# Kernel optimization log

Hardware: AMD Instinct MI355X
Metric: run time of the kernel (lower is better)

## Reference

```python
import jax, jax.numpy as jnp
import numpy as np

N = 100000   # nodes
E = 1600000  # edges (avg degree 16)
DIN, DH, DOUT = 128, 128, 64


def setup_inputs() -> dict:
    key = jax.random.key(0)
    ks = jax.random.split(key, 10)
    x = jax.random.normal(ks[0], (N, DIN), dtype=jnp.float32)
    edge_index = jax.random.randint(ks[1], (2, E), 0, N, dtype=jnp.int32)

    def kaiming(k, fan_out, fan_in):
        # kaiming_uniform_ with nonlinearity='relu': bound = sqrt(6/fan_in)
        bound = np.sqrt(6.0 / fan_in)
        return jax.random.uniform(k, (fan_out, fan_in), jnp.float32, -bound, bound)

    W1 = kaiming(ks[2], DH, DIN)
    W2 = kaiming(ks[3], DH, DH)
    W3 = kaiming(ks[4], DH, DH)
    W4 = kaiming(ks[5], DOUT, DH)
    b1 = jnp.zeros((DH,), jnp.float32)
    b2 = jnp.zeros((DH,), jnp.float32)
    b3 = jnp.zeros((DH,), jnp.float32)
    b4 = jnp.zeros((DOUT,), jnp.float32)
    return {"x": x, "edge_index": edge_index,
            "W1": W1, "b1": b1, "W2": W2, "b2": b2,
            "W3": W3, "b3": b3, "W4": W4, "b4": b4}


def reference(x, edge_index, W1, b1, W2, b2, W3, b3, W4, b4):
    n = x.shape[0]
    src, dst = edge_index[0], edge_index[1]
    # gcn_norm with add_self_loops=False: deg = in-degree at dst (unit weights)
    deg = jax.ops.segment_sum(jnp.ones(src.shape[0], x.dtype), dst, num_segments=n)
    deg_inv_sqrt = jnp.where(deg > 0, jax.lax.rsqrt(jnp.maximum(deg, 1.0)) * jnp.sqrt(jnp.maximum(deg, 1.0)) / jnp.maximum(deg, 1.0) * jnp.sqrt(jnp.maximum(deg, 1.0)), 0.0)
    deg_inv_sqrt = jnp.where(deg > 0, 1.0 / jnp.sqrt(jnp.maximum(deg, 1.0)), 0.0)
    norm = deg_inv_sqrt[src] * deg_inv_sqrt[dst]  # [E]

    def gcn_layer(h, W, b):
        h = h @ W.T                                # [n, out] dense transform
        msg = h[src] * norm[:, None]               # gather + scale  [E, out]
        out = jax.ops.segment_sum(msg, dst, num_segments=n)  # scatter-add
        return out + b

    h = jax.nn.relu(gcn_layer(x, W1, b1))
    h = jax.nn.relu(gcn_layer(h, W2, b2))
    h = jax.nn.relu(gcn_layer(h, W3, b3))
    return gcn_layer(h, W4, b4)
```

## Files before the change

### kernel.cpp

```cpp
#include <hip/hip_runtime.h>
#include <hip/hip_bf16.h>

#define CAP 64
#define BCAP 250000
#define SBCAP 12288

typedef __attribute__((ext_vector_type(8))) short bf16x8;
typedef __attribute__((ext_vector_type(4))) float f32x4;
typedef _Float16 f16;
typedef __attribute__((ext_vector_type(2))) _Float16 f16x2;
typedef __attribute__((ext_vector_type(8))) _Float16 f16x8;

__device__ __forceinline__ ushort f2bf(float f) {
    uint u = __float_as_uint(f);
    u = u + 0x7FFF + ((u >> 16) & 1);
    return (ushort)(u >> 16);
}
__device__ __forceinline__ float bf2f(ushort b) { return __uint_as_float(((uint)b) << 16); }

__device__ __forceinline__ int bkt(int d, int r) {
    int b = 0;
    if (d >= 4 * r) b = 4;
    if (d >= (b + 2) * r) b += 2;
    if (d >= (b + 1) * r) b += 1;
    return b;
}

__global__ __launch_bounds__(256) void route_kernel(const int* __restrict__ src,
                                                    const int* __restrict__ dst,
                                                    int E, int N,
                                                    uint* __restrict__ buf,
                                                    int* __restrict__ gcur8) {
    __shared__ int lcnt[8], lbase[8];
    if (threadIdx.x < 8) lcnt[threadIdx.x] = 0;
    __syncthreads();
    const int r = (N + 7) >> 3;
    const int e = (blockIdx.x * 256 + threadIdx.x) * 4;
    int bb[4]; uint pk[4]; int ne = 0;
    if (e + 4 <= E) {
        int4 d4 = *(const int4*)(dst + e);
        int4 s4 = *(const int4*)(src + e);
        int ds[4] = {d4.x, d4.y, d4.z, d4.w};
        int ss[4] = {s4.x, s4.y, s4.z, s4.w};
#pragma unroll
        for (int k = 0; k < 4; ++k) {
            int b = bkt(ds[k], r);
            bb[k] = b;
            pk[k] = ((uint)ss[k] << 14) | (uint)(ds[k] - b * r);
            atomicAdd(&lcnt[b], 1);
        }
        ne = 4;
    } else {
        for (int t = e; t < E; ++t) {
            int b = bkt(dst[t], r);
            bb[ne] = b;
            pk[ne] = ((uint)src[t] << 14) | (uint)(dst[t] - b * r);
            atomicAdd(&lcnt[b], 1);
            ++ne;
        }
    }
    __syncthreads();
    if (threadIdx.x < 8) {
        lbase[threadIdx.x] = atomicAdd(&gcur8[threadIdx.x], lcnt[threadIdx.x]);
        lcnt[threadIdx.x] = 0;
    }
    __syncthreads();
    for (int k = 0; k < ne; ++k) {
        int idx = lbase[bb[k]] + atomicAdd(&lcnt[bb[k]], 1);
        if (idx < BCAP) buf[(size_t)bb[k] * BCAP + idx] = pk[k];
    }
}

__global__ __launch_bounds__(256) void reroute_kernel(const uint* __restrict__ buf,
                                                      const int* __restrict__ gcur8,
                                                      uint* __restrict__ buf2,
                                                      int* __restrict__ gcur2, int NSUB) {
    __shared__ int lcnt[32], lbase[32];
    const int xg = blockIdx.x & 7;
    const int gidx = blockIdx.x >> 3;
    if (threadIdx.x < NSUB) lcnt[threadIdx.x] = 0;
    __syncthreads();
    int cnt = gcur8[xg];
    if (cnt > BCAP) cnt = BCAP;
    const uint* b = buf + (size_t)xg * BCAP;
    const int e0 = (gidx * 256 + threadIdx.x) * 4;
    uint pk[4]; int sb_[4]; int ne = 0;
    if (e0 + 4 <= cnt) {
        uint4 v = *(const uint4*)(b + e0);
        pk[0] = v.x; pk[1] = v.y; pk[2] = v.z; pk[3] = v.w; ne = 4;
    } else {
        for (int t = e0; t < cnt; ++t) pk[ne++] = b[t];
    }
    for (int k = 0; k < ne; ++k) {
        int sub = (int)(pk[k] & 0x3FFFu) >> 9;
        sb_[k] = sub;
        atomicAdd(&lcnt[sub], 1);
    }
    __syncthreads();
    if (threadIdx.x < NSUB) {
        lbase[threadIdx.x] = atomicAdd(&gcur2[xg * NSUB + threadIdx.x], lcnt[threadIdx.x]);
        lcnt[threadIdx.x] = 0;
    }
    __syncthreads();
    for (int k = 0; k < ne; ++k) {
        int idx = lbase[sb_[k]] + atomicAdd(&lcnt[sb_[k]], 1);
        if (idx < SBCAP) buf2[(size_t)(xg * NSUB + sb_[k]) * SBCAP + idx] = pk[k];
    }
}

__global__ __launch_bounds__(256) void fillsort_kernel(const uint* __restrict__ buf2,
                                                       const int* __restrict__ gcur2,
                                                       int* __restrict__ fil,
                                                       int* __restrict__ csr, int N, int NSUB) {
    __shared__ uint stage[SBCAP];
    __shared__ int lcnt[512];
    const int xg = blockIdx.x & 7;
    const int sub = blockIdx.x >> 3;
    const int sb = xg * NSUB + sub;
    const int r = (N + 7) >> 3;
    const int lo_dl = sub << 9;
    const int ndst = min(512, r - lo_dl);
    if (ndst <= 0) return;
    int cnt = gcur2[sb];
    if (cnt > SBCAP) cnt = SBCAP;
    for (int i = threadIdx.x; i < cnt; i += 256) stage[i] = buf2[(size_t)sb * SBCAP + i];
    for (int i = threadIdx.x; i < ndst; i += 256) lcnt[i] = 0;
    __syncthreads();
    const int lo_d = xg * r + lo_dl;
    for (int i = threadIdx.x; i < cnt; i += 256) {
        uint pk = stage[i];
        int dll = (int)(pk & 0x3FFFu) - lo_dl;
        int s = (int)(pk >> 14);
        int p = atomicAdd(&lcnt[dll], 1);
        if (p < CAP) csr[(size_t)(lo_d + dll) * CAP + p] = s;
    }
    __syncthreads();
    for (int i = threadIdx.x; i < ndst; i += 256) {
        int d = lo_d + i;
        if (d < N) fil[d] = lcnt[i];
    }
}

__global__ void prep_kernel(const float* __restrict__ W1, const float* __restrict__ W2,
                            const float* __restrict__ W3, const float* __restrict__ W4,
                            ushort* __restrict__ hilo,
                            const int* __restrict__ cnt, float* __restrict__ dis, int N) {
    int blk = blockIdx.x;
    if (blk < 224) {
        int i = blk * 256 + threadIdx.x;
        const float* W;
        ushort* hi;
        int off;
        if (i < 16384)      { W = W1; hi = hilo;          off = i; }
        else if (i < 32768) { W = W2; hi = hilo + 32768;  off = i - 16384; }
        else if (i < 49152) { W = W3; hi = hilo + 65536;  off = i - 32768; }
        else                { W = W4; hi = hilo + 98304;  off = i - 49152; }
        float w = W[off];
        ushort h = f2bf(w);
        int span = (i < 49152) ? 16384 : 8192;
        hi[off] = h;
        hi[off + span] = f2bf(w - bf2f(h));
    } else {
        int i = (blk - 224) * 256 + threadIdx.x;
        if (i < N) {
            int c = cnt[i];
            dis[i] = (c > 0) ? rsqrtf((float)c) : 0.0f;
        }
    }
}

template <int COLS, typename FT>
__global__ __launch_bounds__(256) void mfma_gemm_kernel(const FT* __restrict__ F,
                                                        const ushort* __restrict__ Whi,
                                                        const ushort* __restrict__ Wlo,
                                                        const float* __restrict__ dis,
                                                        f16* __restrict__ G, int N) {
    constexpr int CT = COLS / 16;
    const int wave = threadIdx.x >> 6;
    const int lane = threadIdx.x & 63;
    const int lr = lane & 15;
    const int kg = lane >> 4;

    const int rowBase = blockIdx.x * 128 + wave * 32;

    f32x4 acc[2][CT];
#pragma unroll
    for (int rt = 0; rt < 2; ++rt)
#pragma unroll
        for (int c = 0; c < CT; ++c) acc[rt][c] = (f32x4){0.f, 0.f, 0.f, 0.f};

#pragma unroll
    for (int kt = 0; kt < 4; ++kt) {
        bf16x8 Ah[2], Al[2];
#pragma unroll
        for (int rt = 0; rt < 2; ++rt) {
            int row = rowBase + rt * 16 + lr;
            row = row < N ? row : N - 1;
            const FT* p = F + (size_t)row * 128 + kt * 32 + kg * 8;
            float f[8];
            if constexpr (sizeof(FT) == 4) {
                float4 v0 = *(const float4*)p;
                float4 v1 = *(const float4*)(p + 4);
                f[0] = v0.x; f[1] = v0.y; f[2] = v0.z; f[3] = v0.w;
                f[4] = v1.x; f[5] = v1.y; f[6] = v1.z; f[7] = v1.w;
            } else {
                f16x8 v = *(const f16x8*)p;
#pragma unroll
                for (int j = 0; j < 8; ++j) f[j] = (float)v[j];
            }
            bf16x8 h, l;
#pragma unroll
            for (int j = 0; j < 8; ++j) {
                ushort hb = f2bf(f[j]);
                h[j] = (short)hb;
                l[j] = (short)f2bf(f[j] - bf2f(hb));
            }
            Ah[rt] = h;
            Al[rt] = l;
        }
#pragma unroll
        for (int c = 0; c < CT; ++c) {
            const size_t wo = (size_t)(c * 16 + lr) * 128 + kt * 32 + kg * 8;
            bf16x8 Bh = *(const bf16x8*)(Whi + wo);
            bf16x8 Bl = *(const bf16x8*)(Wlo + wo);
#pragma unroll
            for (int rt = 0; rt < 2; ++rt) {
                acc[rt][c] = __builtin_amdgcn_mfma_f32_16x16x32_bf16(Al[rt], Bh, acc[rt][c], 0, 0, 0);
                acc[rt][c] = __builtin_amdgcn_mfma_f32_16x16x32_bf16(Ah[rt], Bl, acc[rt][c], 0, 0, 0);
                acc[rt][c] = __builtin_amdgcn_mfma_f32_16x16x32_bf16(Ah[rt], Bh, acc[rt][c], 0, 0, 0);
            }
        }
    }

#pragma unroll
    for (int rt = 0; rt < 2; ++rt) {
#pragma unroll
        for (int j = 0; j < 4; ++j) {
            int row = rowBase + rt * 16 + kg * 4 + j;
            if (row < N) {
                float d = dis[row];
#pragma unroll
                for (int c = 0; c < CT; ++c)
                    G[(size_t)row * COLS + c * 16 + lr] = (f16)(acc[rt][c][j] * d);
            }
        }
    }
}

template <int WIDTH, bool DO_RELU, typename OT>
__global__ __launch_bounds__(256) void agg_kernel(const f16* __restrict__ g,
                                                  const int* __restrict__ csr,
                                                  const int* __restrict__ cnt,
                                                  const float* __restrict__ dis,
                                                  const float* __restrict__ bias,
                                                  OT* __restrict__ out, int N) {
    constexpr int VPL = WIDTH / 64;
    const int nb8 = gridDim.x >> 3;
    const int vblk = (blockIdx.x & 7) * nb8 + (blockIdx.x >> 3);
    int node = vblk * 4 + (threadIdx.x >> 6);
    if (node >= N) return;
    int lane = threadIdx.x & 63;

    int c = cnt[node];
    if (c > CAP) c = CAP;
    const int* lst = csr + (size_t)node * CAP;
    float acc0 = 0.f, acc1 = 0.f;

    int j = 0;
    for (; j + 8 <= c; j += 8) {
        int4 sA = *(const int4*)(lst + j);
        int4 sB = *(const int4*)(lst + j + 4);
        if (VPL == 2) {
            f16x2 t0 = *(const f16x2*)(g + (size_t)sA.x * WIDTH + lane * 2);
            f16x2 t1 = *(const f16x2*)(g + (size_t)sA.y * WIDTH + lane * 2);
            f16x2 t2 = *(const f16x2*)(g + (size_t)sA.z * WIDTH + lane * 2);
            f16x2 t3 = *(const f16x2*)(g + (size_t)sA.w * WIDTH + lane * 2);
            f16x2 t4 = *(const f16x2*)(g + (size_t)sB.x * WIDTH + lane * 2);
            f16x2 t5 = *(const f16x2*)(g + (size_t)sB.y * WIDTH + lane * 2);
            f16x2 t6 = *(const f16x2*)(g + (size_t)sB.z * WIDTH + lane * 2);
            f16x2 t7 = *(const f16x2*)(g + (size_t)sB.w * WIDTH + lane * 2);
            acc0 += (((float)t0[0] + (float)t1[0]) + ((float)t2[0] + (float)t3[0])) +
                    (((float)t4[0] + (float)t5[0]) + ((float)t6[0] + (float)t7[0]));
            acc1 += (((float)t0[1] + (float)t1[1]) + ((float)t2[1] + (float)t3[1])) +
                    (((float)t4[1] + (float)t5[1]) + ((float)t6[1] + (float)t7[1]));
        } else {
            float u0 = (float)g[(size_t)sA.x * WIDTH + lane];
            float u1 = (float)g[(size_t)sA.y * WIDTH + lane];
            float u2 = (float)g[(size_t)sA.z * WIDTH + lane];
            float u3 = (float)g[(size_t)sA.w * WIDTH + lane];
            float u4 = (float)g[(size_t)sB.x * WIDTH + lane];
            float u5 = (float)g[(size_t)sB.y * WIDTH + lane];
            float u6 = (float)g[(size_t)sB.z * WIDTH + lane];
            float u7 = (float)g[(size_t)sB.w * WIDTH + lane];
            acc0 += ((u0 + u1) + (u2 + u3)) + ((u4 + u5) + (u6 + u7));
        }
    }
    for (; j + 4 <= c; j += 4) {
        int4 sA = *(const int4*)(lst + j);
        if (VPL == 2) {
            f16x2 t0 = *(const f16x2*)(g + (size_t)sA.x * WIDTH + lane * 2);
            f16x2 t1 = *(const f16x2*)(g + (size_t)sA.y * WIDTH + lane * 2);
            f16x2 t2 = *(const f16x2*)(g + (size_t)sA.z * WIDTH + lane * 2);
            f16x2 t3 = *(const f16x2*)(g + (size_t)sA.w * WIDTH + lane * 2);
            acc0 += ((float)t0[0] + (float)t1[0]) + ((float)t2[0] + (float)t3[0]);
            acc1 += ((float)t0[1] + (float)t1[1]) + ((float)t2[1] + (float)t3[1]);
        } else {
            float u0 = (float)g[(size_t)sA.x * WIDTH + lane];
            float u1 = (float)g[(size_t)sA.y * WIDTH + lane];
            float u2 = (float)g[(size_t)sA.z * WIDTH + lane];
            float u3 = (float)g[(size_t)sA.w * WIDTH + lane];
            acc0 += (u0 + u1) + (u2 + u3);
        }
    }
    for (; j < c; ++j) {
        int s = lst[j];
        if (VPL == 2) {
            f16x2 t = *(const f16x2*)(g + (size_t)s * WIDTH + lane * 2);
            acc0 += (float)t[0];
            acc1 += (float)t[1];
        } else {
            acc0 += (float)g[(size_t)s * WIDTH + lane];
        }
    }

    float d = dis[node];
    if (VPL == 2) {
        float v0 = fmaf(d, acc0, bias[lane * 2 + 0]);
        float v1 = fmaf(d, acc1, bias[lane * 2 + 1]);
        if (DO_RELU) { v0 = fmaxf(v0, 0.f); v1 = fmaxf(v1, 0.f); }
        if constexpr (sizeof(OT) == 2) {
            f16x2 o = {(f16)v0, (f16)v1};
            *(f16x2*)(out + (size_t)node * WIDTH + lane * 2) = o;
        } else {
            float2 o = make_float2(v0, v1);
            *(float2*)(out + (size_t)node * WIDTH + lane * 2) = o;
        }
    } else {
        float v0 = fmaf(d, acc0, bias[lane]);
        if (DO_RELU) v0 = fmaxf(v0, 0.f);
        out[(size_t)node * WIDTH + lane] = (OT)v0;
    }
}

extern "C" void kernel_launch(void* const* d_in, const int* in_sizes, int n_in,
                              void* d_out, int out_size, void* d_ws, size_t ws_size,
                              hipStream_t stream) {
    const float* x  = (const float*)d_in[0];
    const int*   ei = (const int*)d_in[1];
    const float* W1 = (const float*)d_in[2];
    const float* b1 = (const float*)d_in[3];
    const float* W2 = (const float*)d_in[4];
    const float* b2 = (const float*)d_in[5];
    const float* W3 = (const float*)d_in[6];
    const float* b3 = (const float*)d_in[7];
    const float* W4 = (const float*)d_in[8];
    const float* b4 = (const float*)d_in[9];

    const int N = in_sizes[0] / 128;
    const int E = in_sizes[1] / 2;
    const int* src = ei;
    const int* dst = ei + E;
    const int r = (N + 7) >> 3;
    const int NSUB = (r + 511) >> 9;

    char* w = (char*)d_ws;
    f16*   F   = (f16*)w;   w += (size_t)N * 128 * 2;
    f16*   G   = (f16*)w;   w += (size_t)N * 128 * 2;
    int*   csr = (int*)w;   w += (size_t)N * CAP * 4;
    float* dis = (float*)w; w += (size_t)N * 4;
    int*   fil = (int*)w;   w += (size_t)N * 4;
    int*   gcur8 = (int*)w; w += 8 * 4;
    int*   gcur2 = (int*)w; w += (size_t)8 * NSUB * 4;
    ushort* Whl = (ushort*)w; w += (16384 * 6 + 8192 * 2) * 2;
    ushort* Whi1 = Whl;          ushort* Wlo1 = Whl + 16384;
    ushort* Whi2 = Whl + 32768;  ushort* Wlo2 = Whl + 49152;
    ushort* Whi3 = Whl + 65536;  ushort* Wlo3 = Whl + 81920;
    ushort* Whi4 = Whl + 98304;  ushort* Wlo4 = Whl + 106496;
    uint* buf  = (uint*)G;
    uint* buf2 = (uint*)G + (size_t)8 * BCAP;

    float* out = (float*)d_out;

    hipMemsetAsync(fil, 0, ((size_t)N + 8 + (size_t)8 * NSUB) * sizeof(int), stream);

    const int nq = (E + 3) / 4;
    route_kernel<<<(nq + 255) / 256, 256, 0, stream>>>(src, dst, E, N, buf, gcur8);
    const int ngrp = ((E / 8) + 1023) / 1024 + 4;
    reroute_kernel<<<8 * ngrp, 256, 0, stream>>>(buf, gcur8, buf2, gcur2, NSUB);
    fillsort_kernel<<<8 * NSUB, 256, 0, stream>>>(buf2, gcur2, fil, csr, N, NSUB);
    prep_kernel<<<224 + (N + 255) / 256, 256, 0, stream>>>(W1, W2, W3, W4, Whl, fil, dis, N);

    const int gemm_grid = (N + 127) / 128;
    const int agg_grid  = (((N + 3) / 4 + 7) / 8) * 8;

    mfma_gemm_kernel<128, float><<<gemm_grid, 256, 0, stream>>>(x, Whi1, Wlo1, dis, G, N);
    agg_kernel<128, true, f16><<<agg_grid, 256, 0, stream>>>(G, csr, fil, dis, b1, F, N);
    mfma_gemm_kernel<128, f16><<<gemm_grid, 256, 0, stream>>>(F, Whi2, Wlo2, dis, G, N);
    agg_kernel<128, true, f16><<<agg_grid, 256, 0, stream>>>(G, csr, fil, dis, b2, F, N);
    mfma_gemm_kernel<128, f16><<<gemm_grid, 256, 0, stream>>>(F, Whi3, Wlo3, dis, G, N);
    agg_kernel<128, true, f16><<<agg_grid, 256, 0, stream>>>(G, csr, fil, dis, b3, F, N);
    mfma_gemm_kernel<64, f16><<<gemm_grid, 256, 0, stream>>>(F, Whi4, Wlo4, dis, G, N);
    agg_kernel<64, false, float><<<agg_grid, 256, 0, stream>>>(G, csr, fil, dis, b4, out, N);
}
```

Baseline: 543.1 us.

## Fuse aggregate-then-transform GCN layers and single-pass edge routing

Reorders the first three layers to aggregate first and then transform. Each layer's gather-sum and the MFMA GEMM now run in one kernel, with the aggregated rows staged in shared memory, and the input is prescaled and converted to fp16 by a new xprep kernel. The two-pass edge bucketing (route, then reroute) is merged into one pass that writes sub-buckets directly. This is meant to remove one intermediate HBM round trip per layer and a kernel launch. The cost is a 32-row fused block whose gather phase may limit occupancy and MFMA efficiency, and more shared-memory atomic bins in the routing kernel.

```diff
diff --git a/kernel.cpp b/kernel.cpp
--- a/kernel.cpp
+++ b/kernel.cpp
@@ -2,7 +2,6 @@
 #include <hip/hip_bf16.h>
 
 #define CAP 64
-#define BCAP 250000
 #define SBCAP 12288
 
 typedef __attribute__((ext_vector_type(8))) short bf16x8;
@@ -29,82 +28,48 @@
 __global__ __launch_bounds__(256) void route_kernel(const int* __restrict__ src,
                                                     const int* __restrict__ dst,
                                                     int E, int N,
-                                                    uint* __restrict__ buf,
-                                                    int* __restrict__ gcur8) {
-    __shared__ int lcnt[8], lbase[8];
-    if (threadIdx.x < 8) lcnt[threadIdx.x] = 0;
+                                                    uint* __restrict__ buf2,
+                                                    int* __restrict__ gcur2, int NSUB) {
+    __shared__ int lcnt[256], lbase[256];
+    const int NS8 = 8 * NSUB;
+    if (threadIdx.x < NS8) lcnt[threadIdx.x] = 0;
     __syncthreads();
     const int r = (N + 7) >> 3;
     const int e = (blockIdx.x * 256 + threadIdx.x) * 4;
-    int bb[4]; uint pk[4]; int ne = 0;
+    int sb_[4]; uint pk[4]; int ne = 0;
     if (e + 4 <= E) {
         int4 d4 = *(const int4*)(dst + e);
         int4 s4 = *(const int4*)(src + e);
-        int ds[4] = {d4.x, d4.y, d4.z, d4.w};
-        int ss[4] = {s4.x, s4.y, s4.z, s4.w};
+        int ds_[4] = {d4.x, d4.y, d4.z, d4.w};
+        int ss_[4] = {s4.x, s4.y, s4.z, s4.w};
 #pragma unroll
         for (int k = 0; k < 4; ++k) {
-            int b = bkt(ds[k], r);
-            bb[k] = b;
-            pk[k] = ((uint)ss[k] << 14) | (uint)(ds[k] - b * r);
-            atomicAdd(&lcnt[b], 1);
+            int b = bkt(ds_[k], r);
+            int dl = ds_[k] - b * r;
+            sb_[k] = b * NSUB + (dl >> 9);
+            pk[k] = ((uint)ss_[k] << 14) | (uint)dl;
+            atomicAdd(&lcnt[sb_[k]], 1);
         }
         ne = 4;
     } else {
         for (int t = e; t < E; ++t) {
             int b = bkt(dst[t], r);
-            bb[ne] = b;
-            pk[ne] = ((uint)src[t] << 14) | (uint)(dst[t] - b * r);
-            atomicAdd(&lcnt[b], 1);
+            int dl = dst[t] - b * r;
+            sb_[ne] = b * NSUB + (dl >> 9);
+            pk[ne] = ((uint)src[t] << 14) | (uint)dl;
+            atomicAdd(&lcnt[sb_[ne]], 1);
             ++ne;
         }
     }
     __syncthreads();
-    if (threadIdx.x < 8) {
-        lbase[threadIdx.x] = atomicAdd(&gcur8[threadIdx.x], lcnt[threadIdx.x]);
-        lcnt[threadIdx.x] = 0;
-    }
-    __syncthreads();
-    for (int k = 0; k < ne; ++k) {
-        int idx = lbase[bb[k]] + atomicAdd(&lcnt[bb[k]], 1);
-        if (idx < BCAP) buf[(size_t)bb[k] * BCAP + idx] = pk[k];
-    }
-}
-
-__global__ __launch_bounds__(256) void reroute_kernel(const uint* __restrict__ buf,
-                                                      const int* __restrict__ gcur8,
-                                                      uint* __restrict__ buf2,
-                                                      int* __restrict__ gcur2, int NSUB) {
-    __shared__ int lcnt[32], lbase[32];
-    const int xg = blockIdx.x & 7;
-    const int gidx = blockIdx.x >> 3;
-    if (threadIdx.x < NSUB) lcnt[threadIdx.x] = 0;
-    __syncthreads();
-    int cnt = gcur8[xg];
-    if (cnt > BCAP) cnt = BCAP;
-    const uint* b = buf + (size_t)xg * BCAP;
-    const int e0 = (gidx * 256 + threadIdx.x) * 4;
-    uint pk[4]; int sb_[4]; int ne = 0;
-    if (e0 + 4 <= cnt) {
-        uint4 v = *(const uint4*)(b + e0);
-        pk[0] = v.x; pk[1] = v.y; pk[2] = v.z; pk[3] = v.w; ne = 4;
-    } else {
-        for (int t = e0; t < cnt; ++t) pk[ne++] = b[t];
-    }
-    for (int k = 0; k < ne; ++k) {
-        int sub = (int)(pk[k] & 0x3FFFu) >> 9;
-        sb_[k] = sub;
-        atomicAdd(&lcnt[sub], 1);
-    }
-    __syncthreads();
-    if (threadIdx.x < NSUB) {
-        lbase[threadIdx.x] = atomicAdd(&gcur2[xg * NSUB + threadIdx.x], lcnt[threadIdx.x]);
+    if (threadIdx.x < NS8) {
+        lbase[threadIdx.x] = atomicAdd(&gcur2[threadIdx.x], lcnt[threadIdx.x]);
         lcnt[threadIdx.x] = 0;
     }
     __syncthreads();
     for (int k = 0; k < ne; ++k) {
         int idx = lbase[sb_[k]] + atomicAdd(&lcnt[sb_[k]], 1);
-        if (idx < SBCAP) buf2[(size_t)(xg * NSUB + sb_[k]) * SBCAP + idx] = pk[k];
+        if (idx < SBCAP) buf2[(size_t)sb_[k] * SBCAP + idx] = pk[k];
     }
 }
 
@@ -169,18 +134,140 @@
     }
 }
 
-template <int COLS, typename FT>
-__global__ __launch_bounds__(256) void mfma_gemm_kernel(const FT* __restrict__ F,
-                                                        const ushort* __restrict__ Whi,
-                                                        const ushort* __restrict__ Wlo,
-                                                        const float* __restrict__ dis,
-                                                        f16* __restrict__ G, int N) {
-    constexpr int CT = COLS / 16;
+__global__ __launch_bounds__(256) void xprep_kernel(const float* __restrict__ x,
+                                                    const int* __restrict__ cnt,
+                                                    f16* __restrict__ h0, int N) {
+    int q = blockIdx.x * 256 + threadIdx.x;
+    if (q * 4 >= N * 128) return;
+    int row = q >> 5;
+    int c = cnt[row];
+    float dd = (c > 0) ? rsqrtf((float)c) : 0.0f;
+    float4 v = *(const float4*)(x + (size_t)q * 4);
+    f16 o[4] = {(f16)(v.x * dd), (f16)(v.y * dd), (f16)(v.z * dd), (f16)(v.w * dd)};
+    *(f16x2*)(h0 + (size_t)q * 4) = (f16x2){o[0], o[1]};
+    *(f16x2*)(h0 + (size_t)q * 4 + 2) = (f16x2){o[2], o[3]};
+}
+
+template <bool DO_RELU>
+__global__ __launch_bounds__(256) void fused_kernel(const f16* __restrict__ hin,
+                                                    const ushort* __restrict__ Whi,
+                                                    const ushort* __restrict__ Wlo,
+                                                    const int* __restrict__ csr,
+                                                    const int* __restrict__ cnt,
+                                                    const float* __restrict__ dis,
+                                                    const float* __restrict__ bias,
+                                                    f16* __restrict__ hout, int N) {
+    __shared__ float a[32][132];
+    const int wave = threadIdx.x >> 6;
+    const int lane = threadIdx.x & 63;
+    const int nb8 = gridDim.x >> 3;
+    const int vblk = (blockIdx.x & 7) * nb8 + (blockIdx.x >> 3);
+    const int rowBase = vblk * 32;
+
+    for (int k = 0; k < 8; ++k) {
+        const int nl = wave * 8 + k;
+        const int node = rowBase + nl;
+        float acc0 = 0.f, acc1 = 0.f;
+        if (node < N) {
+            int c = cnt[node];
+            if (c > CAP) c = CAP;
+            const int* lst = csr + (size_t)node * CAP;
+            int j = 0;
+            for (; j + 8 <= c; j += 8) {
+                int4 sA = *(const int4*)(lst + j);
+                int4 sB = *(const int4*)(lst + j + 4);
+                f16x2 t0 = *(const f16x2*)(hin + (size_t)sA.x * 128 + lane * 2);
+                f16x2 t1 = *(const f16x2*)(hin + (size_t)sA.y * 128 + lane * 2);
+                f16x2 t2 = *(const f16x2*)(hin + (size_t)sA.z * 128 + lane * 2);
+                f16x2 t3 = *(const f16x2*)(hin + (size_t)sA.w * 128 + lane * 2);
+                f16x2 t4 = *(const f16x2*)(hin + (size_t)sB.x * 128 + lane * 2);
+                f16x2 t5 = *(const f16x2*)(hin + (size_t)sB.y * 128 + lane * 2);
+                f16x2 t6 = *(const f16x2*)(hin + (size_t)sB.z * 128 + lane * 2);
+                f16x2 t7 = *(const f16x2*)(hin + (size_t)sB.w * 128 + lane * 2);
+                acc0 += (((float)t0[0] + (float)t1[0]) + ((float)t2[0] + (float)t3[0])) +
+                        (((float)t4[0] + (float)t5[0]) + ((float)t6[0] + (float)t7[0]));
+                acc1 += (((float)t0[1] + (float)t1[1]) + ((float)t2[1] + (float)t3[1])) +
+                        (((float)t4[1] + (float)t5[1]) + ((float)t6[1] + (float)t7[1]));
+            }
+            for (; j + 4 <= c; j += 4) {
+                int4 sA = *(const int4*)(lst + j);
+                f16x2 t0 = *(const f16x2*)(hin + (size_t)sA.x * 128 + lane * 2);
+                f16x2 t1 = *(const f16x2*)(hin + (size_t)sA.y * 128 + lane * 2);
+                f16x2 t2 = *(const f16x2*)(hin + (size_t)sA.z * 128 + lane * 2);
+                f16x2 t3 = *(const f16x2*)(hin + (size_t)sA.w * 128 + lane * 2);
+                acc0 += ((float)t0[0] + (float)t1[0]) + ((float)t2[0] + (float)t3[0]);
+                acc1 += ((float)t0[1] + (float)t1[1]) + ((float)t2[1] + (float)t3[1]);
+            }
+            for (; j < c; ++j) {
+                int s = lst[j];
+                f16x2 t = *(const f16x2*)(hin + (size_t)s * 128 + lane * 2);
+                acc0 += (float)t[0];
+                acc1 += (float)t[1];
+            }
+            float dd = dis[node];
+            acc0 *= dd;
+            acc1 *= dd;
+        }
+        *(float2*)(&a[nl][lane * 2]) = make_float2(acc0, acc1);
+    }
+    __syncthreads();
+
+    const int lr = lane & 15;
+    const int kg = lane >> 4;
+    const int rt = wave & 1;
+    const int ctb = (wave >> 1) * 4;
+    f32x4 acc[4];
+#pragma unroll
+    for (int c = 0; c < 4; ++c) acc[c] = (f32x4){0.f, 0.f, 0.f, 0.f};
+
+#pragma unroll
+    for (int kt = 0; kt < 4; ++kt) {
+        float f[8];
+#pragma unroll
+        for (int j = 0; j < 8; ++j) f[j] = a[rt * 16 + lr][kt * 32 + kg * 8 + j];
+        bf16x8 Ah, Al;
+#pragma unroll
+        for (int j = 0; j < 8; ++j) {
+            ushort hb = f2bf(f[j]);
+            Ah[j] = (short)hb;
+            Al[j] = (short)f2bf(f[j] - bf2f(hb));
+        }
+#pragma unroll
+        for (int c = 0; c < 4; ++c) {
+            const size_t wo = (size_t)((ctb + c) * 16 + lr) * 128 + kt * 32 + kg * 8;
+            bf16x8 Bh = *(const bf16x8*)(Whi + wo);
+            bf16x8 Bl = *(const bf16x8*)(Wlo + wo);
+            acc[c] = __builtin_amdgcn_mfma_f32_16x16x32_bf16(Al, Bh, acc[c], 0, 0, 0);
+            acc[c] = __builtin_amdgcn_mfma_f32_16x16x32_bf16(Ah, Bl, acc[c], 0, 0, 0);
+            acc[c] = __builtin_amdgcn_mfma_f32_16x16x32_bf16(Ah, Bh, acc[c], 0, 0, 0);
+        }
+    }
+
+#pragma unroll
+    for (int j = 0; j < 4; ++j) {
+        int row = rowBase + rt * 16 + kg * 4 + j;
+        if (row < N) {
+            float dd = dis[row];
+#pragma unroll
+            for (int c = 0; c < 4; ++c) {
+                int col = (ctb + c) * 16 + lr;
+                float v = acc[c][j] + bias[col];
+                if (DO_RELU) v = fmaxf(v, 0.f);
+                hout[(size_t)row * 128 + col] = (f16)(v * dd);
+            }
+        }
+    }
+}
+
+__global__ __launch_bounds__(256) void gemm64_kernel(const f16* __restrict__ F,
+                                                     const ushort* __restrict__ Whi,
+                                                     const ushort* __restrict__ Wlo,
+                                                     f16* __restrict__ G, int N) {
+    constexpr int CT = 4;
     const int wave = threadIdx.x >> 6;
     const int lane = threadIdx.x & 63;
     const int lr = lane & 15;
     const int kg = lane >> 4;
-
     const int rowBase = blockIdx.x * 128 + wave * 32;
 
     f32x4 acc[2][CT];
@@ -196,24 +283,14 @@
         for (int rt = 0; rt < 2; ++rt) {
             int row = rowBase + rt * 16 + lr;
             row = row < N ? row : N - 1;
-            const FT* p = F + (size_t)row * 128 + kt * 32 + kg * 8;
-            float f[8];
-            if constexpr (sizeof(FT) == 4) {
-                float4 v0 = *(const float4*)p;
-                float4 v1 = *(const float4*)(p + 4);
-                f[0] = v0.x; f[1] = v0.y; f[2] = v0.z; f[3] = v0.w;
-                f[4] = v1.x; f[5] = v1.y; f[6] = v1.z; f[7] = v1.w;
-            } else {
-                f16x8 v = *(const f16x8*)p;
-#pragma unroll
-                for (int j = 0; j < 8; ++j) f[j] = (float)v[j];
-            }
+            f16x8 v = *(const f16x8*)(F + (size_t)row * 128 + kt * 32 + kg * 8);
             bf16x8 h, l;
 #pragma unroll
             for (int j = 0; j < 8; ++j) {
-                ushort hb = f2bf(f[j]);
+                float fv = (float)v[j];
+                ushort hb = f2bf(fv);
                 h[j] = (short)hb;
-                l[j] = (short)f2bf(f[j] - bf2f(hb));
+                l[j] = (short)f2bf(fv - bf2f(hb));
             }
             Ah[rt] = h;
             Al[rt] = l;
@@ -231,30 +308,24 @@
             }
         }
     }
-
-#pragma unroll
-    for (int rt = 0; rt < 2; ++rt) {
+#pragma unroll
+    for (int rt = 0; rt < 2; ++rt)
 #pragma unroll
         for (int j = 0; j < 4; ++j) {
             int row = rowBase + rt * 16 + kg * 4 + j;
-            if (row < N) {
-                float d = dis[row];
+            if (row < N)
 #pragma unroll
                 for (int c = 0; c < CT; ++c)
-                    G[(size_t)row * COLS + c * 16 + lr] = (f16)(acc[rt][c][j] * d);
-            }
-        }
-    }
-}
-
-template <int WIDTH, bool DO_RELU, typename OT>
-__global__ __launch_bounds__(256) void agg_kernel(const f16* __restrict__ g,
-                                                  const int* __restrict__ csr,
-                                                  const int* __restrict__ cnt,
-                                                  const float* __restrict__ dis,
-                                                  const float* __restrict__ bias,
-                                                  OT* __restrict__ out, int N) {
-    constexpr int VPL = WIDTH / 64;
+                    G[(size_t)row * 64 + c * 16 + lr] = (f16)acc[rt][c][j];
+        }
+}
+
+__global__ __launch_bounds__(256) void agg64_kernel(const f16* __restrict__ g,
+                                                    const int* __restrict__ csr,
+                                                    const int* __restrict__ cnt,
+                                                    const float* __restrict__ dis,
+                                                    const float* __restrict__ bias,
+                                                    float* __restrict__ out, int N) {
     const int nb8 = gridDim.x >> 3;
     const int vblk = (blockIdx.x & 7) * nb8 + (blockIdx.x >> 3);
     int node = vblk * 4 + (threadIdx.x >> 6);
@@ -264,82 +335,34 @@
     int c = cnt[node];
     if (c > CAP) c = CAP;
     const int* lst = csr + (size_t)node * CAP;
-    float acc0 = 0.f, acc1 = 0.f;
+    float acc0 = 0.f;
 
     int j = 0;
     for (; j + 8 <= c; j += 8) {
         int4 sA = *(const int4*)(lst + j);
         int4 sB = *(const int4*)(lst + j + 4);
-        if (VPL == 2) {
-            f16x2 t0 = *(const f16x2*)(g + (size_t)sA.x * WIDTH + lane * 2);
-            f16x2 t1 = *(const f16x2*)(g + (size_t)sA.y * WIDTH + lane * 2);
-            f16x2 t2 = *(const f16x2*)(g + (size_t)sA.z * WIDTH + lane * 2);
-            f16x2 t3 = *(const f16x2*)(g + (size_t)sA.w * WIDTH + lane * 2);
-            f16x2 t4 = *(const f16x2*)(g + (size_t)sB.x * WIDTH + lane * 2);
-            f16x2 t5 = *(const f16x2*)(g + (size_t)sB.y * WIDTH + lane * 2);
-            f16x2 t6 = *(const f16x2*)(g + (size_t)sB.z * WIDTH + lane * 2);
-            f16x2 t7 = *(const f16x2*)(g + (size_t)sB.w * WIDTH + lane * 2);
-            acc0 += (((float)t0[0] + (float)t1[0]) + ((float)t2[0] + (float)t3[0])) +
-                    (((float)t4[0] + (float)t5[0]) + ((float)t6[0] + (float)t7[0]));
-            acc1 += (((float)t0[1] + (float)t1[1]) + ((float)t2[1] + (float)t3[1])) +
-                    (((float)t4[1] + (float)t5[1]) + ((float)t6[1] + (float)t7[1]));
-        } else {
-            float u0 = (float)g[(size_t)sA.x * WIDTH + lane];
-            float u1 = (float)g[(size_t)sA.y * WIDTH + lane];
-            float u2 = (float)g[(size_t)sA.z * WIDTH + lane];
-            float u3 = (float)g[(size_t)sA.w * WIDTH + lane];
-            float u4 = (float)g[(size_t)sB.x * WIDTH + lane];
-            float u5 = (float)g[(size_t)sB.y * WIDTH + lane];
-            float u6 = (float)g[(size_t)sB.z * WIDTH + lane];
-            float u7 = (float)g[(size_t)sB.w * WIDTH + lane];
-            acc0 += ((u0 + u1) + (u2 + u3)) + ((u4 + u5) + (u6 + u7));
-        }
+        float u0 = (float)g[(size_t)sA.x * 64 + lane];
+        float u1 = (float)g[(size_t)sA.y * 64 + lane];
+        float u2 = (float)g[(size_t)sA.z * 64 + lane];
+        float u3 = (float)g[(size_t)sA.w * 64 + lane];
+        float u4 = (float)g[(size_t)sB.x * 64 + lane];
+        float u5 = (float)g[(size_t)sB.y * 64 + lane];
+        float u6 = (float)g[(size_t)sB.z * 64 + lane];
+        float u7 = (float)g[(size_t)sB.w * 64 + lane];
+        acc0 += ((u0 + u1) + (u2 + u3)) + ((u4 + u5) + (u6 + u7));
     }
     for (; j + 4 <= c; j += 4) {
         int4 sA = *(const int4*)(lst + j);
-        if (VPL == 2) {
-            f16x2 t0 = *(const f16x2*)(g + (size_t)sA.x * WIDTH + lane * 2);
-            f16x2 t1 = *(const f16x2*)(g + (size_t)sA.y * WIDTH + lane * 2);
-            f16x2 t2 = *(const f16x2*)(g + (size_t)sA.z * WIDTH + lane * 2);
-            f16x2 t3 = *(const f16x2*)(g + (size_t)sA.w * WIDTH + lane * 2);
-            acc0 += ((float)t0[0] + (float)t1[0]) + ((float)t2[0] + (float)t3[0]);
-            acc1 += ((float)t0[1] + (float)t1[1]) + ((float)t2[1] + (float)t3[1]);
-        } else {
-            float u0 = (float)g[(size_t)sA.x * WIDTH + lane];
-            float u1 = (float)g[(size_t)sA.y * WIDTH + lane];
-            float u2 = (float)g[(size_t)sA.z * WIDTH + lane];
-            float u3 = (float)g[(size_t)sA.w * WIDTH + lane];
-            acc0 += (u0 + u1) + (u2 + u3);
-        }
-    }
-    for (; j < c; ++j) {
-        int s = lst[j];
-        if (VPL == 2) {
-            f16x2 t = *(const f16x2*)(g + (size_t)s * WIDTH + lane * 2);
-            acc0 += (float)t[0];
-            acc1 += (float)t[1];
-        } else {
-            acc0 += (float)g[(size_t)s * WIDTH + lane];
-        }
-    }
-
-    float d = dis[node];
-    if (VPL == 2) {
-        float v0 = fmaf(d, acc0, bias[lane * 2 + 0]);
-        float v1 = fmaf(d, acc1, bias[lane * 2 + 1]);
-        if (DO_RELU) { v0 = fmaxf(v0, 0.f); v1 = fmaxf(v1, 0.f); }
-        if constexpr (sizeof(OT) == 2) {
-            f16x2 o = {(f16)v0, (f16)v1};
-            *(f16x2*)(out + (size_t)node * WIDTH + lane * 2) = o;
-        } else {
-            float2 o = make_float2(v0, v1);
-            *(float2*)(out + (size_t)node * WIDTH + lane * 2) = o;
-        }
-    } else {
-        float v0 = fmaf(d, acc0, bias[lane]);
-        if (DO_RELU) v0 = fmaxf(v0, 0.f);
-        out[(size_t)node * WIDTH + lane] = (OT)v0;
-    }
+        float u0 = (float)g[(size_t)sA.x * 64 + lane];
+        float u1 = (float)g[(size_t)sA.y * 64 + lane];
+        float u2 = (float)g[(size_t)sA.z * 64 + lane];
+        float u3 = (float)g[(size_t)sA.w * 64 + lane];
+        acc0 += (u0 + u1) + (u2 + u3);
+    }
+    for (; j < c; ++j) acc0 += (float)g[(size_t)lst[j] * 64 + lane];
+
+    float v0 = fmaf(dis[node], acc0, bias[lane]);
+    out[(size_t)node * 64 + lane] = v0;
 }
 
 extern "C" void kernel_launch(void* const* d_in, const int* in_sizes, int n_in,
@@ -362,43 +385,38 @@
     const int* dst = ei + E;
     const int r = (N + 7) >> 3;
     const int NSUB = (r + 511) >> 9;
+    const int NS8 = 8 * NSUB;
 
     char* w = (char*)d_ws;
-    f16*   F   = (f16*)w;   w += (size_t)N * 128 * 2;
-    f16*   G   = (f16*)w;   w += (size_t)N * 128 * 2;
+    f16*   H0  = (f16*)w;   w += (size_t)N * 128 * 2;
+    f16*   H1  = (f16*)w;   w += (size_t)N * 128 * 2;
     int*   csr = (int*)w;   w += (size_t)N * CAP * 4;
     float* dis = (float*)w; w += (size_t)N * 4;
     int*   fil = (int*)w;   w += (size_t)N * 4;
-    int*   gcur8 = (int*)w; w += 8 * 4;
-    int*   gcur2 = (int*)w; w += (size_t)8 * NSUB * 4;
+    int*   gcur2 = (int*)w; w += (size_t)NS8 * 4;
     ushort* Whl = (ushort*)w; w += (16384 * 6 + 8192 * 2) * 2;
     ushort* Whi1 = Whl;          ushort* Wlo1 = Whl + 16384;
     ushort* Whi2 = Whl + 32768;  ushort* Wlo2 = Whl + 49152;
     ushort* Whi3 = Whl + 65536;  ushort* Wlo3 = Whl + 81920;
     ushort* Whi4 = Whl + 98304;  ushort* Wlo4 = Whl + 106496;
-    uint* buf  = (uint*)G;
-    uint* buf2 = (uint*)G + (size_t)8 * BCAP;
+    uint* buf2 = (uint*)H1;
+    f16*  G4   = H0;
 
     float* out = (float*)d_out;
 
-    hipMemsetAsync(fil, 0, ((size_t)N + 8 + (size_t)8 * NSUB) * sizeof(int), stream);
-
-    const int nq = (E + 3) / 4;
-    route_kernel<<<(nq + 255) / 256, 256, 0, stream>>>(src, dst, E, N, buf, gcur8);
-    const int ngrp = ((E / 8) + 1023) / 1024 + 4;
-    reroute_kernel<<<8 * ngrp, 256, 0, stream>>>(buf, gcur8, buf2, gcur2, NSUB);
+    hipMemsetAsync(fil, 0, ((size_t)N + NS8) * sizeof(int), stream);
+
+    route_kernel<<<((E + 3) / 4 + 255) / 256, 256, 0, stream>>>(src, dst, E, N, buf2, gcur2, NSUB);
     fillsort_kernel<<<8 * NSUB, 256, 0, stream>>>(buf2, gcur2, fil, csr, N, NSUB);
     prep_kernel<<<224 + (N + 255) / 256, 256, 0, stream>>>(W1, W2, W3, W4, Whl, fil, dis, N);
-
-    const int gemm_grid = (N + 127) / 128;
-    const int agg_grid  = (((N + 3) / 4 + 7) / 8) * 8;
-
-    mfma_gemm_kernel<128, float><<<gemm_grid, 256, 0, stream>>>(x, Whi1, Wlo1, dis, G, N);
-    agg_kernel<128, true, f16><<<agg_grid, 256, 0, stream>>>(G, csr, fil, dis, b1, F, N);
-    mfma_gemm_kernel<128, f16><<<gemm_grid, 256, 0, stream>>>(F, Whi2, Wlo2, dis, G, N);
-    agg_kernel<128, true, f16><<<agg_grid, 256, 0, stream>>>(G, csr, fil, dis, b2, F, N);
-    mfma_gemm_kernel<128, f16><<<gemm_grid, 256, 0, stream>>>(F, Whi3, Wlo3, dis, G, N);
-    agg_kernel<128, true, f16><<<agg_grid, 256, 0, stream>>>(G, csr, fil, dis, b3, F, N);
-    mfma_gemm_kernel<64, f16><<<gemm_grid, 256, 0, stream>>>(F, Whi4, Wlo4, dis, G, N);
-    agg_kernel<64, false, float><<<agg_grid, 256, 0, stream>>>(G, csr, fil, dis, b4, out, N);
-}
+    xprep_kernel<<<((N * 128 / 4) + 255) / 256, 256, 0, stream>>>(x, fil, H0, N);
+
+    const int fgrid = (((N + 31) / 32 + 7) / 8) * 8;
+    const int agrid = (((N + 3) / 4 + 7) / 8) * 8;
+
+    fused_kernel<true><<<fgrid, 256, 0, stream>>>(H0, Whi1, Wlo1, csr, fil, dis, b1, H1, N);
+    fused_kernel<true><<<fgrid, 256, 0, stream>>>(H1, Whi2, Wlo2, csr, fil, dis, b2, H0, N);
+    fused_kernel<true><<<fgrid, 256, 0, stream>>>(H0, Whi3, Wlo3, csr, fil, dis, b3, H1, N);
+    gemm64_kernel<<<(N + 127) / 128, 256, 0, stream>>>(H1, Whi4, Wlo4, G4, N);
+    agg64_kernel<<<agrid, 256, 0, stream>>>(G4, csr, fil, dis, b4, out, N);
+}
```

Result: slower. 624.8 us (+15.0%).
